# Kernel tuning notes

Hardware: AMD Instinct MI355X
Metric: run time of the kernel (lower is better)

## Reference

```python
import jax, jax.numpy as jnp
import numpy as np

NEG_SLOPE = 0.2  # PyG GATConv default negative_slope


def _gat_conv(h, src, dst, N, W, a_src, a_dst, b, heads):
    """PyG GATConv (eval mode, self-loops already in src/dst).
    h: [N, F_in], W: [F_in, heads*C], a_src/a_dst: [heads, C], b: [heads*C]."""
    C = W.shape[1] // heads
    hl = (h @ W).reshape(N, heads, C)                      # [N,H,C]
    al_s = jnp.einsum('nhc,hc->nh', hl, a_src)             # [N,H]
    al_d = jnp.einsum('nhc,hc->nh', hl, a_dst)             # [N,H]
    e = jax.nn.leaky_relu(al_s[src] + al_d[dst], NEG_SLOPE)  # [E,H]
    # segment softmax over incoming edges of each destination node
    m = jax.ops.segment_max(e, dst, num_segments=N)        # [N,H]
    ex = jnp.exp(e - m[dst])
    s = jax.ops.segment_sum(ex, dst, num_segments=N)
    alpha = ex / (s[dst] + 1e-16)                          # [E,H]
    out = jax.ops.segment_sum(hl[src] * alpha[:, :, None], dst, num_segments=N)
    return out.reshape(N, heads * C) + b


def setup_inputs() -> dict:
    key = jax.random.key(0)
    ks = jax.random.split(key, 16)
    N, E, D = 30000, 240000, 64
    NUM_ENT, NUM_REL, NUM_DRUGS = 100000, 64, 200
    sc = 0.1
    return {
        'x': jax.random.randint(ks[0], (N,), 0, NUM_ENT),
        'edge_index': jax.random.randint(ks[1], (2, E), 0, N),
        'edge_type': jax.random.randint(ks[2], (N,), 0, NUM_REL),
        'ent_emb': jax.random.normal(ks[3], (NUM_ENT, D), jnp.float32) * sc,
        'rel_emb': jax.random.normal(ks[4], (NUM_REL, D), jnp.float32) * sc,
        'W1': jax.random.normal(ks[5], (2 * D, 8 * D), jnp.float32) * sc,
        'att1_src': jax.random.normal(ks[6], (8, D), jnp.float32) * sc,
        'att1_dst': jax.random.normal(ks[7], (8, D), jnp.float32) * sc,
        'b1': jax.random.normal(ks[8], (8 * D,), jnp.float32) * sc,
        'W2': jax.random.normal(ks[9], (9 * D, D), jnp.float32) * sc,
        'att2_src': jax.random.normal(ks[10], (1, D), jnp.float32) * sc,
        'att2_dst': jax.random.normal(ks[11], (1, D), jnp.float32) * sc,
        'b2': jax.random.normal(ks[12], (D,), jnp.float32) * sc,
        'fc_w': jax.random.normal(ks[13], (D, NUM_DRUGS), jnp.float32) * sc,
        'fc_b': jax.random.normal(ks[14], (NUM_DRUGS,), jnp.float32) * sc,
    }


def reference(x, edge_index, edge_type, ent_emb, rel_emb, W1, att1_src, att1_dst, b1,
              W2, att2_src, att2_dst, b2, fc_w, fc_b):
    N = x.shape[0]
    loop = jnp.arange(N)
    src = jnp.concatenate([edge_index[0], loop])  # GATConv add_self_loops=True
    dst = jnp.concatenate([edge_index[1], loop])
    ent = ent_emb[x]                               # [N,D]
    rel = rel_emb[edge_type]                       # [N,D]
    h = jnp.concatenate([ent, rel], axis=-1)       # [N,2D]  (dropout is identity in eval)
    h = jax.nn.elu(_gat_conv(h, src, dst, N, W1, att1_src, att1_dst, b1, heads=8))  # [N,8D]
    h = jnp.concatenate([h, ent], axis=-1)         # [N,9D]
    h = jax.nn.elu(_gat_conv(h, src, dst, N, W2, att2_src, att2_dst, b2, heads=1))  # [N,D]
    g = jnp.mean(h, axis=0, keepdims=True)         # [1,D]
    return g @ fc_w + fc_b                         # [1,num_drugs]
```

## Files before the change

### kernel.cpp

```cpp
#include <hip/hip_runtime.h>
#include <math.h>

#define NEG_SLOPE 0.2f

typedef __attribute__((ext_vector_type(8))) short short8;
typedef __attribute__((ext_vector_type(4))) float f32x4;
typedef __attribute__((ext_vector_type(2))) float f32x2;

__device__ __forceinline__ float lrelu(float v) { return v > 0.f ? v : NEG_SLOPE * v; }
__device__ __forceinline__ float elu(float v) { return v > 0.f ? v : (__expf(v) - 1.f); }
__device__ __forceinline__ unsigned short f2b(float f) {
    unsigned u = __float_as_uint(f);
    return (unsigned short)((u + 0x7FFFu + ((u >> 16) & 1u)) >> 16);
}
__device__ __forceinline__ unsigned packb(float a, float b) {
    return ((unsigned)f2b(b) << 16) | (unsigned)f2b(a);
}
__device__ __forceinline__ unsigned short pack8(float a, float b) {
    return (unsigned short)(__builtin_amdgcn_cvt_pk_fp8_f32(a, b, 0, false) & 0xFFFF);
}
__device__ __forceinline__ f32x2 unpack8(unsigned v) {
    return __builtin_amdgcn_cvt_pk_f32_fp8((int)v, false);
}
__device__ __forceinline__ f32x2 unpack8hi(unsigned v) {
    return __builtin_amdgcn_cvt_pk_f32_fp8((int)v, true);
}
__device__ __forceinline__ unsigned bpack_trunc(f32x2 f) {
    return (__float_as_uint(f.y) & 0xFFFF0000u) | (__float_as_uint(f.x) >> 16);
}
__device__ __forceinline__ int sw(int r, int o) { return (o ^ (r & 7)) << 3; }

__global__ void prep_k(const int* __restrict__ x, const int* __restrict__ et,
                       const int* __restrict__ ei,
                       const float* __restrict__ ent_emb, const float* __restrict__ rel_emb,
                       const float* __restrict__ W1, const float* __restrict__ W2,
                       unsigned* __restrict__ h1b2, unsigned short* __restrict__ W1t,
                       unsigned short* __restrict__ W2t, unsigned char* __restrict__ h2q8,
                       int* __restrict__ deg, int N, int E) {
    int t = blockIdx.x * blockDim.x + threadIdx.x;
    if (t < N * 64) {
        int n = t >> 6, j = t & 63;
        float v0, v1;
        if (j < 32) {
            const float* e = ent_emb + (size_t)x[n] * 64 + 2 * j;
            v0 = e[0]; v1 = e[1];
            *(unsigned short*)(h2q8 + (size_t)n * 576 + 512 + 2 * j) = pack8(v0, v1);
        } else {
            const float* r = rel_emb + (size_t)et[n] * 64 + 2 * (j - 32);
            v0 = r[0]; v1 = r[1];
        }
        h1b2[t] = packb(v0, v1);
    }
    if (t < 512 * 128) {
        int n = t >> 7, kk = t & 127;
        W1t[t] = f2b(W1[(size_t)kk * 512 + n]);
    }
    if (t < 64 * 576) {
        int n = t / 576, k = t % 576;
        W2t[t] = f2b(W2[(size_t)k * 64 + n]);
    }
    if (t < E + N) {
        int dst = t < E ? ei[E + t] : t - E;
        atomicAdd(&deg[dst], 1);
    }
}

__global__ __launch_bounds__(256) void scan_k(const int* __restrict__ deg,
                                              int* __restrict__ offs,
                                              int* __restrict__ bstate,
                                              int N, int Etot, int NB) {
    __shared__ int s[256];
    __shared__ int sbase;
    int b = blockIdx.x, t = threadIdx.x;
    int i = b * 256 + t;
    int v = (i < N) ? deg[i] : 0;
    s[t] = v;
    __syncthreads();
    for (int off = 1; off < 256; off <<= 1) {
        int tmp = (t >= off) ? s[t - off] : 0;
        __syncthreads();
        s[t] += tmp;
        __syncthreads();
    }
    int total = s[255];
    if (t == 0) {
        if (b == 0) {
            atomicExch(&bstate[0], (total << 2) | 2);
            sbase = 0;
        } else {
            atomicExch(&bstate[b], (total << 2) | 1);
            int run = 0;
            for (int p = b - 1; p >= 0;) {
                int stv;
                do { stv = atomicAdd(&bstate[p], 0); } while ((stv & 3) == 0);
                run += (stv >> 2);
                if ((stv & 3) == 2) break;
                p--;
            }
            atomicExch(&bstate[b], ((run + total) << 2) | 2);
            sbase = run;
        }
    }
    __syncthreads();
    if (i < N) offs[i] = sbase + s[t] - v;
    if (b == NB - 1 && t == 0) offs[N] = Etot;
}

__global__ void fill_k(const int* __restrict__ ei, int E, int N,
                       const int* __restrict__ offs, int* __restrict__ cursor,
                       int* __restrict__ csr) {
    int e = blockIdx.x * blockDim.x + threadIdx.x;
    if (e >= E + N) return;
    int src = e < E ? ei[e] : e - E;
    int dst = e < E ? ei[E + e] : e - E;
    int pos = offs[dst] + atomicAdd(&cursor[dst], 1);
    csr[pos] = src;
}

__global__ __launch_bounds__(256) void gemm1_k(const unsigned short* __restrict__ A,
                                               const unsigned short* __restrict__ W1t,
                                               const float* __restrict__ a1s,
                                               const float* __restrict__ a1d,
                                               unsigned char* __restrict__ hl8,
                                               float* __restrict__ als, float* __restrict__ ald,
                                               int M) {
    __shared__ __align__(16) unsigned short As[128 * 128];
    __shared__ __align__(16) unsigned short Bs[64 * 128];
    int tid = threadIdx.x;
    int m0 = blockIdx.x * 128, h = blockIdx.y;
    for (int c = tid; c < 2048; c += 256) {
        int r = c >> 4, o = c & 15;
        int gr = m0 + r;
        uint4 v = make_uint4(0u, 0u, 0u, 0u);
        if (gr < M) v = *(const uint4*)(A + (size_t)gr * 128 + o * 8);
        *(uint4*)(As + r * 128 + sw(r, o)) = v;
    }
    for (int c = tid; c < 1024; c += 256) {
        int r = c >> 4, o = c & 15;
        uint4 v = *(const uint4*)(W1t + (size_t)(h * 64 + r) * 128 + o * 8);
        *(uint4*)(Bs + r * 128 + sw(r, o)) = v;
    }
    __syncthreads();
    int w = tid >> 6, lane = tid & 63;
    int wr = w * 32;
    int m16 = lane & 15, quad = lane >> 4;
    f32x4 acc[2][4] = {};
#pragma unroll
    for (int kk = 0; kk < 128; kk += 32) {
        int ob = (kk >> 3) + quad;
        short8 b[4];
#pragma unroll
        for (int j = 0; j < 4; j++) {
            int r = j * 16 + m16;
            b[j] = *(const short8*)(Bs + r * 128 + sw(r, ob));
        }
#pragma unroll
        for (int i = 0; i < 2; i++) {
            int r = wr + i * 16 + m16;
            short8 a = *(const short8*)(As + r * 128 + sw(r, ob));
#pragma unroll
            for (int j = 0; j < 4; j++)
                acc[i][j] = __builtin_amdgcn_mfma_f32_16x16x32_bf16(a, b[j], acc[i][j], 0, 0, 0);
        }
    }
#pragma unroll
    for (int i = 0; i < 2; i++)
#pragma unroll
        for (int j = 0; j < 4; j++)
#pragma unroll
            for (int reg = 0; reg < 4; reg++) {
                int row = m0 + wr + i * 16 + quad * 4 + reg;
                int col = h * 64 + j * 16 + m16;
                if (row < M)
                    hl8[(size_t)row * 512 + col] =
                        (unsigned char)(__builtin_amdgcn_cvt_pk_fp8_f32(acc[i][j][reg] * 8.f,
                                                                        0.f, 0, false) & 0xFF);
            }
    float sa[2][4] = {}, sd[2][4] = {};
#pragma unroll
    for (int j = 0; j < 4; j++) {
        int col = h * 64 + j * 16 + m16;
        float ws_ = a1s[col], wd_ = a1d[col];
#pragma unroll
        for (int i = 0; i < 2; i++)
#pragma unroll
            for (int reg = 0; reg < 4; reg++) {
                sa[i][reg] += acc[i][j][reg] * ws_;
                sd[i][reg] += acc[i][j][reg] * wd_;
            }
    }
#pragma unroll
    for (int m = 1; m < 16; m <<= 1)
#pragma unroll
        for (int i = 0; i < 2; i++)
#pragma unroll
            for (int reg = 0; reg < 4; reg++) {
                sa[i][reg] += __shfl_xor(sa[i][reg], m, 64);
                sd[i][reg] += __shfl_xor(sd[i][reg], m, 64);
            }
    if (m16 == 0)
#pragma unroll
        for (int i = 0; i < 2; i++)
#pragma unroll
            for (int reg = 0; reg < 4; reg++) {
                int row = m0 + wr + i * 16 + quad * 4 + reg;
                if (row < M) { als[row * 8 + h] = sa[i][reg]; ald[row * 8 + h] = sd[i][reg]; }
            }
}

#define ACCP(e_, u_)                                      \
    {                                                     \
        f32x2 g0 = unpack8(u_.x), g1 = unpack8hi(u_.x);   \
        f32x2 g2 = unpack8(u_.y), g3 = unpack8hi(u_.y);   \
        acc[0] += (e_) * g0.x; acc[1] += (e_) * g0.y;     \
        acc[2] += (e_) * g1.x; acc[3] += (e_) * g1.y;     \
        acc[4] += (e_) * g2.x; acc[5] += (e_) * g2.y;     \
        acc[6] += (e_) * g3.x; acc[7] += (e_) * g3.y;     \
    }

__global__ __launch_bounds__(256) void agg1_k(const unsigned char* __restrict__ hl8,
                                              const float* __restrict__ als1,
                                              const float* __restrict__ ald1,
                                              const float* __restrict__ b1,
                                              const int* __restrict__ offs,
                                              const int* __restrict__ csr,
                                              unsigned char* __restrict__ h2q8, int N) {
    int wv = threadIdx.x >> 6;
    int t = threadIdx.x & 63;
    int n = blockIdx.x * 4 + wv;
    if (n >= N) return;
    int h = t >> 3;
    float dl = ald1[n * 8 + h];
    int p0 = offs[n], p1 = offs[n + 1];
    float acc[8] = {};
    float ssum = 0.f;
    int p = p0;
    for (; p + 4 <= p1; p += 4) {
        int sA = csr[p], sB = csr[p + 1], sC = csr[p + 2], sD = csr[p + 3];
        float eA = __expf(lrelu(als1[sA * 8 + h] + dl));
        float eB = __expf(lrelu(als1[sB * 8 + h] + dl));
        float eC = __expf(lrelu(als1[sC * 8 + h] + dl));
        float eD = __expf(lrelu(als1[sD * 8 + h] + dl));
        uint2 vA = *(const uint2*)(hl8 + (size_t)sA * 512 + t * 8);
        uint2 vB = *(const uint2*)(hl8 + (size_t)sB * 512 + t * 8);
        uint2 vC = *(const uint2*)(hl8 + (size_t)sC * 512 + t * 8);
        uint2 vD = *(const uint2*)(hl8 + (size_t)sD * 512 + t * 8);
        ssum += (eA + eB) + (eC + eD);
        ACCP(eA, vA);
        ACCP(eB, vB);
        ACCP(eC, vC);
        ACCP(eD, vD);
    }
    for (; p < p1; p++) {
        int sA = csr[p];
        float eA = __expf(lrelu(als1[sA * 8 + h] + dl));
        uint2 vA = *(const uint2*)(hl8 + (size_t)sA * 512 + t * 8);
        ssum += eA;
        ACCP(eA, vA);
    }
    float iv = 0.125f / (ssum + 1e-16f);
    float4 bq0 = *(const float4*)(b1 + t * 8);
    float4 bq1 = *(const float4*)(b1 + t * 8 + 4);
    float r0 = elu(acc[0] * iv + bq0.x);
    float r1 = elu(acc[1] * iv + bq0.y);
    float r2 = elu(acc[2] * iv + bq0.z);
    float r3 = elu(acc[3] * iv + bq0.w);
    float r4 = elu(acc[4] * iv + bq1.x);
    float r5 = elu(acc[5] * iv + bq1.y);
    float r6 = elu(acc[6] * iv + bq1.z);
    float r7 = elu(acc[7] * iv + bq1.w);
    uint2 o;
    int d0 = __builtin_amdgcn_cvt_pk_fp8_f32(r0, r1, 0, false);
    o.x = (unsigned)__builtin_amdgcn_cvt_pk_fp8_f32(r2, r3, d0, true);
    int d1 = __builtin_amdgcn_cvt_pk_fp8_f32(r4, r5, 0, false);
    o.y = (unsigned)__builtin_amdgcn_cvt_pk_fp8_f32(r6, r7, d1, true);
    *(uint2*)(h2q8 + (size_t)n * 576 + t * 8) = o;
}

__global__ __launch_bounds__(256) void gemm2_k(const unsigned char* __restrict__ Aq8,
                                               const unsigned short* __restrict__ Bt,
                                               const float* __restrict__ a2s,
                                               const float* __restrict__ a2d,
                                               unsigned char* __restrict__ hl2q,
                                               float* __restrict__ als2,
                                               float* __restrict__ ald2, int M) {
    __shared__ __align__(16) unsigned short As[64 * 64];
    __shared__ __align__(16) unsigned short Bs[64 * 64];
    int tid = threadIdx.x;
    int m0 = blockIdx.x * 64;
    int w = tid >> 6, lane = tid & 63;
    int m16 = lane & 15, quad = lane >> 4;
    f32x4 acc[4] = {};
    for (int k0 = 0; k0 < 576; k0 += 64) {
        __syncthreads();
        {
            int r = tid >> 2, o = tid & 3;
            int gr = m0 + r;
            uint4 v = make_uint4(0u, 0u, 0u, 0u);
            if (gr < M) v = *(const uint4*)(Aq8 + (size_t)gr * 576 + k0 + o * 16);
            uint4 w0, w1;
            w0.x = bpack_trunc(unpack8(v.x));   w0.y = bpack_trunc(unpack8hi(v.x));
            w0.z = bpack_trunc(unpack8(v.y));   w0.w = bpack_trunc(unpack8hi(v.y));
            w1.x = bpack_trunc(unpack8(v.z));   w1.y = bpack_trunc(unpack8hi(v.z));
            w1.z = bpack_trunc(unpack8(v.w));   w1.w = bpack_trunc(unpack8hi(v.w));
            *(uint4*)(As + r * 64 + sw(r, 2 * o)) = w0;
            *(uint4*)(As + r * 64 + sw(r, 2 * o + 1)) = w1;
        }
        for (int c = tid; c < 512; c += 256) {
            int r = c >> 3, o = c & 7;
            uint4 v = *(const uint4*)(Bt + (size_t)r * 576 + k0 + o * 8);
            *(uint4*)(Bs + r * 64 + sw(r, o)) = v;
        }
        __syncthreads();
#pragma unroll
        for (int kk = 0; kk < 64; kk += 32) {
            int ob = (kk >> 3) + quad;
            int r = w * 16 + m16;
            short8 a = *(const short8*)(As + r * 64 + sw(r, ob));
#pragma unroll
            for (int j = 0; j < 4; j++) {
                int rb = j * 16 + m16;
                short8 b = *(const short8*)(Bs + rb * 64 + sw(rb, ob));
                acc[j] = __builtin_amdgcn_mfma_f32_16x16x32_bf16(a, b, acc[j], 0, 0, 0);
            }
        }
    }
#pragma unroll
    for (int j = 0; j < 4; j++)
#pragma unroll
        for (int reg = 0; reg < 4; reg++) {
            int row = m0 + w * 16 + quad * 4 + reg;
            int col = j * 16 + m16;
            if (row < M)
                hl2q[(size_t)row * 64 + col] =
                    (unsigned char)(__builtin_amdgcn_cvt_pk_fp8_f32(acc[j][reg], 0.f, 0, false) & 0xFF);
        }
    float sa[4] = {}, sd[4] = {};
#pragma unroll
    for (int j = 0; j < 4; j++) {
        int col = j * 16 + m16;
        float as_ = a2s[col], ad_ = a2d[col];
#pragma unroll
        for (int reg = 0; reg < 4; reg++) {
            sa[reg] += acc[j][reg] * as_;
            sd[reg] += acc[j][reg] * ad_;
        }
    }
#pragma unroll
    for (int m = 1; m < 16; m <<= 1)
#pragma unroll
        for (int reg = 0; reg < 4; reg++) {
            sa[reg] += __shfl_xor(sa[reg], m, 64);
            sd[reg] += __shfl_xor(sd[reg], m, 64);
        }
    if (m16 == 0)
#pragma unroll
        for (int reg = 0; reg < 4; reg++) {
            int row = m0 + w * 16 + quad * 4 + reg;
            if (row < M) { als2[row] = sa[reg]; ald2[row] = sd[reg]; }
        }
}

__global__ __launch_bounds__(256) void agg2_k(const unsigned short* __restrict__ hl2q16,
                                              const float* __restrict__ als2,
                                              const float* __restrict__ ald2,
                                              const float* __restrict__ b2,
                                              const int* __restrict__ offs,
                                              const int* __restrict__ csr,
                                              float* __restrict__ gpart, int N) {
    __shared__ float red[512];
    int slot = threadIdx.x >> 5, l = threadIdx.x & 31;
    int n = blockIdx.x * 8 + slot;
    float v0 = 0.f, v1 = 0.f;
    if (n < N) {
        float dl = ald2[n];
        int p0 = offs[n], p1 = offs[n + 1];
        float a0 = 0.f, a1 = 0.f, ssum = 0.f;
        int p = p0;
        for (; p + 1 < p1; p += 2) {
            int sA = csr[p], sB = csr[p + 1];
            float lA = als2[sA], lB = als2[sB];
            unsigned hA = hl2q16[sA * 32 + l];
            unsigned hB = hl2q16[sB * 32 + l];
            float xA = __expf(lrelu(lA + dl));
            float xB = __expf(lrelu(lB + dl));
            ssum += xA + xB;
            f32x2 fA = unpack8(hA), fB = unpack8(hB);
            a0 += xA * fA.x + xB * fB.x;
            a1 += xA * fA.y + xB * fB.y;
        }
        if (p < p1) {
            int sA = csr[p];
            float xA = __expf(lrelu(als2[sA] + dl));
            ssum += xA;
            f32x2 fA = unpack8(hl2q16[sA * 32 + l]);
            a0 += xA * fA.x;
            a1 += xA * fA.y;
        }
        float inv = 1.f / (ssum + 1e-16f);
        v0 = elu(a0 * inv + b2[2 * l]);
        v1 = elu(a1 * inv + b2[2 * l + 1]);
    }
    red[slot * 64 + 2 * l] = v0;
    red[slot * 64 + 2 * l + 1] = v1;
    __syncthreads();
    if (threadIdx.x < 64) {
        float s = 0.f;
#pragma unroll
        for (int ss = 0; ss < 8; ss++) s += red[ss * 64 + threadIdx.x];
        gpart[(size_t)blockIdx.x * 64 + threadIdx.x] = s;
    }
}

__global__ __launch_bounds__(256) void colredfinal_k(const float* __restrict__ gpart,
                                                     float* __restrict__ gsum,
                                                     int* __restrict__ done,
                                                     const float* __restrict__ fcw,
                                                     const float* __restrict__ fcb,
                                                     float* __restrict__ out,
                                                     int NBL, int N, int NCB) {
    __shared__ float red[256];
    __shared__ int isLast;
    int t = threadIdx.x;
    int c = t & 63, rg = t >> 6;
    int bend = blockIdx.x * 256 + 256; if (bend > NBL) bend = NBL;
    float acc = 0.f;
    for (int b = blockIdx.x * 256 + rg; b < bend; b += 4)
        acc += gpart[(size_t)b * 64 + c];
    red[t] = acc;
    __syncthreads();
    if (t < 64) atomicAdd(&gsum[c], red[c] + red[c + 64] + red[c + 128] + red[c + 192]);
    __threadfence();
    if (t == 0) {
        int old = atomicAdd(done, 1);
        isLast = (old == NCB - 1) ? 1 : 0;
    }
    __syncthreads();
    if (isLast) {
        __shared__ float g[64];
        if (t < 64) g[t] = atomicAdd(&gsum[t], 0.f) / (float)N;
        __syncthreads();
        if (t < 200) {
            float a = fcb[t];
#pragma unroll
            for (int cc = 0; cc < 64; cc++) a += g[cc] * fcw[cc * 200 + t];
            out[t] = a;
        }
    }
}

extern "C" void kernel_launch(void* const* d_in, const int* in_sizes, int n_in,
                              void* d_out, int out_size, void* d_ws, size_t ws_size,
                              hipStream_t stream) {
    const int* x = (const int*)d_in[0];
    const int* ei = (const int*)d_in[1];
    const int* et = (const int*)d_in[2];
    const float* ent_emb = (const float*)d_in[3];
    const float* rel_emb = (const float*)d_in[4];
    const float* W1 = (const float*)d_in[5];
    const float* a1s = (const float*)d_in[6];
    const float* a1d = (const float*)d_in[7];
    const float* b1 = (const float*)d_in[8];
    const float* W2 = (const float*)d_in[9];
    const float* a2s = (const float*)d_in[10];
    const float* a2d = (const float*)d_in[11];
    const float* b2 = (const float*)d_in[12];
    const float* fcw = (const float*)d_in[13];
    const float* fcb = (const float*)d_in[14];
    float* out = (float*)d_out;

    int N = in_sizes[0];
    int E = in_sizes[1] / 2;
    int Etot = E + N;
    int NB = (N + 255) / 256;
    int NBL = (N + 7) / 8;
    int NCB = (NBL + 255) / 256;

    char* p = (char*)d_ws;
    auto alloc = [&](size_t bytes) -> char* {
        char* r = p;
        p += (bytes + 255) & ~(size_t)255;
        return r;
    };
    unsigned* h1b2 = (unsigned*)alloc((size_t)N * 64 * 4);
    unsigned short* W1t = (unsigned short*)alloc((size_t)512 * 128 * 2);
    unsigned short* W2t = (unsigned short*)alloc((size_t)64 * 576 * 2);
    float* als1 = (float*)alloc((size_t)N * 8 * 4);
    float* ald1 = (float*)alloc((size_t)N * 8 * 4);
    unsigned char* hl8 = (unsigned char*)alloc((size_t)N * 512);
    unsigned char* h2q8 = (unsigned char*)alloc((size_t)N * 576);
    unsigned char* hl2q = (unsigned char*)alloc((size_t)N * 64);
    float* als2 = (float*)alloc((size_t)N * 4);
    float* ald2 = (float*)alloc((size_t)N * 4);
    float* gpart = (float*)alloc((size_t)NBL * 64 * 4);
    int* offs   = (int*)alloc((size_t)(N + 1) * 4);
    int* csr    = (int*)alloc((size_t)Etot * 4);
    char* z0 = p;
    int* deg    = (int*)alloc((size_t)N * 4);
    int* cursor = (int*)alloc((size_t)N * 4);
    float* gsum = (float*)alloc(64 * 4);
    int* done   = (int*)alloc(4);
    int* bstate = (int*)alloc((size_t)NB * 4);
    size_t zbytes = (size_t)(p - z0);

    int tb = 256;
    hipMemsetAsync(z0, 0, zbytes, stream);
    prep_k<<<(N * 64 + tb - 1) / tb, tb, 0, stream>>>(x, et, ei, ent_emb, rel_emb,
                                                      W1, W2, h1b2, W1t, W2t, h2q8, deg, N, E);
    scan_k<<<NB, 256, 0, stream>>>(deg, offs, bstate, N, Etot, NB);
    fill_k<<<(Etot + tb - 1) / tb, tb, 0, stream>>>(ei, E, N, offs, cursor, csr);
    gemm1_k<<<dim3((N + 127) / 128, 8), 256, 0, stream>>>((const unsigned short*)h1b2, W1t,
                                                          a1s, a1d, hl8, als1, ald1, N);
    agg1_k<<<(N + 3) / 4, 256, 0, stream>>>(hl8, als1, ald1, b1, offs, csr, h2q8, N);
    gemm2_k<<<(N + 63) / 64, 256, 0, stream>>>(h2q8, W2t, a2s, a2d, hl2q, als2, ald2, N);
    agg2_k<<<NBL, 256, 0, stream>>>((const unsigned short*)hl2q, als2, ald2, b2, offs, csr, gpart, N);
    colredfinal_k<<<NCB, 256, 0, stream>>>(gpart, gsum, done, fcw, fcb, out, NBL, N, NCB);
}
```

Before: 241.5 us.

## Merge CSR fill and first GEMM into one launch for concurrent execution

Combines the edge CSR fill kernel and the layer-1 GEMM into a single grid. The first FB blocks do the atomic scatter of edges and the rest compute GEMM tiles, with the head index taken from the flattened block id. The two pieces of work are independent, so this removes one launch and lets the memory-bound scatter overlap the compute-bound GEMM. In exchange, the fill blocks now carry the GEMM kernel's large shared-memory allocation, which may lower how many fill blocks can be resident at once.

```diff
diff --git a/kernel.cpp b/kernel.cpp
--- a/kernel.cpp
+++ b/kernel.cpp
@@ -106,28 +106,36 @@
     if (b == NB - 1 && t == 0) offs[N] = Etot;
 }
 
-__global__ void fill_k(const int* __restrict__ ei, int E, int N,
-                       const int* __restrict__ offs, int* __restrict__ cursor,
-                       int* __restrict__ csr) {
-    int e = blockIdx.x * blockDim.x + threadIdx.x;
-    if (e >= E + N) return;
-    int src = e < E ? ei[e] : e - E;
-    int dst = e < E ? ei[E + e] : e - E;
-    int pos = offs[dst] + atomicAdd(&cursor[dst], 1);
-    csr[pos] = src;
-}
-
-__global__ __launch_bounds__(256) void gemm1_k(const unsigned short* __restrict__ A,
-                                               const unsigned short* __restrict__ W1t,
-                                               const float* __restrict__ a1s,
-                                               const float* __restrict__ a1d,
-                                               unsigned char* __restrict__ hl8,
-                                               float* __restrict__ als, float* __restrict__ ald,
-                                               int M) {
+__global__ __launch_bounds__(256) void fillgemm1_k(const int* __restrict__ ei, int E, int N,
+                                                   const int* __restrict__ offs,
+                                                   int* __restrict__ cursor,
+                                                   int* __restrict__ csr,
+                                                   const unsigned short* __restrict__ A,
+                                                   const unsigned short* __restrict__ W1t,
+                                                   const float* __restrict__ a1s,
+                                                   const float* __restrict__ a1d,
+                                                   unsigned char* __restrict__ hl8,
+                                                   float* __restrict__ als,
+                                                   float* __restrict__ ald,
+                                                   int FB, int NMB) {
     __shared__ __align__(16) unsigned short As[128 * 128];
     __shared__ __align__(16) unsigned short Bs[64 * 128];
+    int bid = blockIdx.x;
     int tid = threadIdx.x;
-    int m0 = blockIdx.x * 128, h = blockIdx.y;
+    if (bid < FB) {
+        int e = bid * 256 + tid;
+        if (e < E + N) {
+            int src = e < E ? ei[e] : e - E;
+            int dst = e < E ? ei[E + e] : e - E;
+            int pos = offs[dst] + atomicAdd(&cursor[dst], 1);
+            csr[pos] = src;
+        }
+        return;
+    }
+    int g = bid - FB;
+    int h = g / NMB, mb = g - h * NMB;
+    int m0 = mb * 128;
+    int M = N;
     for (int c = tid; c < 2048; c += 256) {
         int r = c >> 4, o = c & 15;
         int gr = m0 + r;
@@ -475,6 +483,8 @@
     int NB = (N + 255) / 256;
     int NBL = (N + 7) / 8;
     int NCB = (NBL + 255) / 256;
+    int FB = (Etot + 255) / 256;
+    int NMB = (N + 127) / 128;
 
     char* p = (char*)d_ws;
     auto alloc = [&](size_t bytes) -> char* {
@@ -508,9 +518,9 @@
     prep_k<<<(N * 64 + tb - 1) / tb, tb, 0, stream>>>(x, et, ei, ent_emb, rel_emb,
                                                       W1, W2, h1b2, W1t, W2t, h2q8, deg, N, E);
     scan_k<<<NB, 256, 0, stream>>>(deg, offs, bstate, N, Etot, NB);
-    fill_k<<<(Etot + tb - 1) / tb, tb, 0, stream>>>(ei, E, N, offs, cursor, csr);
-    gemm1_k<<<dim3((N + 127) / 128, 8), 256, 0, stream>>>((const unsigned short*)h1b2, W1t,
-                                                          a1s, a1d, hl8, als1, ald1, N);
+    fillgemm1_k<<<FB + NMB * 8, 256, 0, stream>>>(ei, E, N, offs, cursor, csr,
+                                                  (const unsigned short*)h1b2, W1t,
+                                                  a1s, a1d, hl8, als1, ald1, FB, NMB);
     agg1_k<<<(N + 3) / 4, 256, 0, stream>>>(hl8, als1, ald1, b1, offs, csr, h2q8, N);
     gemm2_k<<<(N + 63) / 64, 256, 0, stream>>>(h2q8, W2t, a2s, a2d, hl2q, als2, ald2, N);
     agg2_k<<<NBL, 256, 0, stream>>>((const unsigned short*)hl2q, als2, ald2, b2, offs, csr, gpart, N);
```

New measurement: 234.5 us. 1.03x faster.
